# Kernel tuning notes

Hardware: AMD Instinct MI355X
Metric: run time of the kernel (lower is better)

## Reference

```python
import jax, jax.numpy as jnp
import numpy as np
from jax import lax

S = 8192      # total tokens
HID = 1280    # hidden_size
H = 16        # num_heads
D = HID // H  # head_dim = 80
NSEG = 8      # number of equal-length segments (images)


def rotate_half(x):
    half = x.shape[-1] // 2
    return jnp.concatenate([-x[..., half:], x[..., :half]], axis=-1)


def setup_inputs() -> dict:
    key = jax.random.key(0)
    k1, k2, k3, k4 = jax.random.split(key, 4)
    hidden_states = jax.random.normal(k1, (S, HID), dtype=jnp.float32)
    # rotary embeddings: angles repeated over both halves, as in standard vision RoPE
    theta = jax.random.uniform(k2, (S, D // 2), dtype=jnp.float32) * (2.0 * np.pi)
    freqs = jnp.concatenate([theta, theta], axis=-1)  # [S, D]
    cos = jnp.cos(freqs)
    sin = jnp.sin(freqs)
    qkv_kernel = jax.random.normal(k3, (HID, 3, H, D), dtype=jnp.float32) * 0.02
    qkv_bias = jnp.zeros((3, H, D), dtype=jnp.float32)
    proj_kernel = jax.random.normal(k4, (H * D, HID), dtype=jnp.float32) * 0.02
    proj_bias = jnp.zeros((HID,), dtype=jnp.float32)
    cu_seqlens = jnp.arange(NSEG + 1, dtype=jnp.int32) * (S // NSEG)
    return {
        "hidden_states": hidden_states, "cos": cos, "sin": sin,
        "qkv_kernel": qkv_kernel, "qkv_bias": qkv_bias,
        "proj_kernel": proj_kernel, "proj_bias": proj_bias,
        "cu_seqlens": cu_seqlens,
    }


def reference(hidden_states, cos, sin, qkv_kernel, qkv_bias, proj_kernel, proj_bias, cu_seqlens):
    P = lax.Precision.HIGHEST
    seq, dtype = hidden_states.shape[0], hidden_states.dtype
    # fused QKV projection: [S, 3, H, D]
    qkv = jnp.einsum('sd,dtnh->stnh', hidden_states, qkv_kernel, precision=P) + qkv_bias
    q, k, v = qkv[:, 0], qkv[:, 1], qkv[:, 2]
    # rotary position embedding in fp32 (as in original)
    cf = cos[:, None, :].astype(jnp.float32)
    sf = sin[:, None, :].astype(jnp.float32)
    qf = q.astype(jnp.float32)
    kf = k.astype(jnp.float32)
    q = (qf * cf + rotate_half(qf) * sf).astype(dtype)
    k = (kf * cf + rotate_half(kf) * sf).astype(dtype)
    # block-diagonal attention over equal-length segments from cu_seqlens
    n_seg = cu_seqlens.shape[0] - 1
    L = seq // n_seg  # segment length (uniform segments)
    head_dim = q.shape[-1]
    scale = head_dim ** (-0.5)
    qs = q.reshape(n_seg, L, H, head_dim)
    ks = k.reshape(n_seg, L, H, head_dim)
    vs = v.reshape(n_seg, L, H, head_dim)
    logits = jnp.einsum('bqhd,bkhd->bhqk', qs, ks, precision=P) * scale
    attn = jax.nn.softmax(logits.astype(jnp.float32), axis=-1).astype(dtype)
    out = jnp.einsum('bhqk,bkhd->bqhd', attn, vs, precision=P).reshape(seq, H * head_dim)
    return jnp.einsum('se,ed->sd', out, proj_kernel, precision=P) + proj_bias
```

## Files before the change

### kernel.cpp

```cpp
#include <hip/hip_runtime.h>

#define S_LEN 8192
#define HID   1280
#define NHEAD 16
#define HD    80
#define NQKV  3840
#define VTS   8256

#define GLOBAL_AS __attribute__((address_space(1)))
#define LDS_AS    __attribute__((address_space(3)))

typedef __attribute__((ext_vector_type(8))) short bf16x8;
typedef __attribute__((ext_vector_type(4))) float f32x4;
typedef __attribute__((ext_vector_type(4))) unsigned short u16x4;
typedef __attribute__((ext_vector_type(8))) unsigned short u16x8;
typedef __attribute__((ext_vector_type(2))) unsigned int u32x2;

__device__ __forceinline__ unsigned short f2bf(float f) {
    union { float f; unsigned int u; } v; v.f = f;
    unsigned int r = v.u + 0x7FFFu + ((v.u >> 16) & 1u);
    return (unsigned short)(r >> 16);
}
__device__ __forceinline__ float bf2f(unsigned short h) {
    union { unsigned int u; float f; } v; v.u = ((unsigned int)h) << 16;
    return v.f;
}
__device__ __forceinline__ unsigned int cvt_pk_bf16(float a, float b) {
    unsigned int r;
    asm("v_cvt_pk_bf16_f32 %0, %1, %2" : "=v"(r) : "v"(a), "v"(b));
    return r;
}

__global__ __launch_bounds__(256) void k_cvt(const float* __restrict__ src,
                                             unsigned short* __restrict__ dst, int n4)
{
    int i = blockIdx.x * 256 + threadIdx.x;
    if (i >= n4) return;
    f32x4 v = *(const f32x4*)&src[(size_t)i * 4];
    u16x4 o;
    o[0] = f2bf(v[0]); o[1] = f2bf(v[1]); o[2] = f2bf(v[2]); o[3] = f2bf(v[3]);
    *(u16x4*)&dst[(size_t)i * 4] = o;
}

__global__ __launch_bounds__(256) void k_wt(const float* __restrict__ W,
                                            unsigned short* __restrict__ Wt,
                                            int R, int C)
{
    __shared__ float T[32][33];
    int r0 = blockIdx.y * 32, c0 = blockIdx.x * 32;
    int tr = threadIdx.x >> 3, tc = (threadIdx.x & 7) * 4;
    f32x4 v = *(const f32x4*)&W[(size_t)(r0 + tr) * C + c0 + tc];
    T[tr][tc + 0] = v[0]; T[tr][tc + 1] = v[1];
    T[tr][tc + 2] = v[2]; T[tr][tc + 3] = v[3];
    __syncthreads();
    int c = threadIdx.x >> 3, r4 = (threadIdx.x & 7) * 4;
    u16x4 o;
    o[0] = f2bf(T[r4 + 0][c]); o[1] = f2bf(T[r4 + 1][c]);
    o[2] = f2bf(T[r4 + 2][c]); o[3] = f2bf(T[r4 + 3][c]);
    *(u16x4*)&Wt[(size_t)(c0 + c) * R + r0 + r4] = o;
}

__global__ __launch_bounds__(256) void k_vtr(const unsigned short* __restrict__ vb,
                                             unsigned short* __restrict__ vt)
{
    const int b = blockIdx.x;
    const int h = b >> 6, s0 = (b & 63) * 128;
    const int tid = threadIdx.x;
    if (tid >= 160) return;
    const int sblk = tid & 15, dch = tid >> 4;
    u16x8 a[8];
#pragma unroll
    for (int j = 0; j < 8; ++j)
        a[j] = *(const u16x8*)&vb[(size_t)(s0 + sblk * 8 + j) * HID + h * HD + dch * 8];
#pragma unroll
    for (int jj = 0; jj < 8; ++jj) {
        u16x8 o;
#pragma unroll
        for (int j = 0; j < 8; ++j) o[j] = a[j][jj];
        *(u16x8*)&vt[(size_t)(h * HD + dch * 8 + jj) * VTS + s0 + sblk * 8] = o;
    }
}

__global__ __launch_bounds__(512, 2) void k_qkv256(
    const unsigned short* __restrict__ A,
    const unsigned short* __restrict__ Bt,
    const float* __restrict__ bias,
    unsigned short* __restrict__ q0, unsigned short* __restrict__ k0p,
    unsigned short* __restrict__ v0)
{
    __shared__ __align__(16) unsigned short As[2][2][16][64][8];
    __shared__ __align__(16) unsigned short Bs[2][2][16][64][8];
    const int tid = threadIdx.x;
    const int w = tid >> 6, l = tid & 63;
    const int qg = l & 15, g = l >> 4;
    const int wm = w >> 2, wn = w & 3;
    const int wm8 = wm * 8, wn4 = wn * 4;

    const int bid = blockIdx.x;
    const int xcd = bid & 7, t = bid >> 3;
    const int bm0 = (xcd * 4 + (t & 3)) * 256;
    const int bn0 = (t >> 2) * 256;

    const unsigned short* ga = A + (size_t)(bm0 + w * 16 + qg) * HID + g * 8;
    const unsigned short* gb = Bt + (size_t)(bn0 + w * 16 + qg) * HID + g * 8;

#define SG_A(d, ks, kcol) do {                                                  \
    __builtin_amdgcn_global_load_lds((const GLOBAL_AS unsigned int*)(ga + (kcol)), \
        (LDS_AS unsigned int*)&As[d][ks][w][0][0], 16, 0, 0);                   \
    __builtin_amdgcn_global_load_lds((const GLOBAL_AS unsigned int*)(ga + (size_t)128 * HID + (kcol)), \
        (LDS_AS unsigned int*)&As[d][ks][8 + w][0][0], 16, 0, 0); } while (0)
#define SG_B(d, ks, kcol) do {                                                  \
    __builtin_amdgcn_global_load_lds((const GLOBAL_AS unsigned int*)(gb + (kcol)), \
        (LDS_AS unsigned int*)&Bs[d][ks][w][0][0], 16, 0, 0);                   \
    __builtin_amdgcn_global_load_lds((const GLOBAL_AS unsigned int*)(gb + (size_t)128 * HID + (kcol)), \
        (LDS_AS unsigned int*)&Bs[d][ks][8 + w][0][0], 16, 0, 0); } while (0)

#define RD_A4(d, ks, fb) do {                                                   \
    af[0] = *(const bf16x8*)&As[d][ks][wm8 + (fb) + 0][l][0];                   \
    af[1] = *(const bf16x8*)&As[d][ks][wm8 + (fb) + 1][l][0];                   \
    af[2] = *(const bf16x8*)&As[d][ks][wm8 + (fb) + 2][l][0];                   \
    af[3] = *(const bf16x8*)&As[d][ks][wm8 + (fb) + 3][l][0]; } while (0)
#define RD_B4(d, ks) do {                                                       \
    bf[0] = *(const bf16x8*)&Bs[d][ks][wn4 + 0][l][0];                          \
    bf[1] = *(const bf16x8*)&Bs[d][ks][wn4 + 1][l][0];                          \
    bf[2] = *(const bf16x8*)&Bs[d][ks][wn4 + 2][l][0];                          \
    bf[3] = *(const bf16x8*)&Bs[d][ks][wn4 + 3][l][0]; } while (0)

#define MFMAQ(base) do {                                                        \
    _Pragma("unroll")                                                           \
    for (int m = 0; m < 4; ++m)                                                 \
        _Pragma("unroll")                                                       \
        for (int n = 0; n < 4; ++n)                                             \
            acc[(base) + m][n] = __builtin_amdgcn_mfma_f32_16x16x32_bf16(       \
                af[m], bf[n], acc[(base) + m][n], 0, 0, 0); } while (0)

#define BARW() do { __builtin_amdgcn_s_barrier();                               \
    asm volatile("s_waitcnt lgkmcnt(0)" ::: "memory");                          \
    __builtin_amdgcn_sched_barrier(0);                                          \
    __builtin_amdgcn_s_setprio(1); } while (0)
#define BARC() do { __builtin_amdgcn_s_setprio(0);                              \
    __builtin_amdgcn_s_barrier();                                               \
    __builtin_amdgcn_sched_barrier(0); } while (0)
#define BARC_VM4() do { __builtin_amdgcn_s_setprio(0);                          \
    asm volatile("s_waitcnt vmcnt(4)" ::: "memory");                            \
    __builtin_amdgcn_s_barrier();                                               \
    __builtin_amdgcn_sched_barrier(0); } while (0)
#define BARC_VM0() do { __builtin_amdgcn_s_setprio(0);                          \
    asm volatile("s_waitcnt vmcnt(0)" ::: "memory");                            \
    __builtin_amdgcn_s_barrier();                                               \
    __builtin_amdgcn_sched_barrier(0); } while (0)

    f32x4 acc[8][4];
#pragma unroll
    for (int m = 0; m < 8; ++m)
#pragma unroll
        for (int n = 0; n < 4; ++n) acc[m][n] = (f32x4){0.f, 0.f, 0.f, 0.f};

    SG_A(0, 0, 0);  SG_B(0, 0, 0);
    SG_A(0, 1, 32); SG_B(0, 1, 32);
    SG_A(1, 0, 64); SG_B(1, 0, 64);
    asm volatile("s_waitcnt vmcnt(4)" ::: "memory");
    __builtin_amdgcn_s_barrier();
    __builtin_amdgcn_sched_barrier(0);

    const int NIT = HID / 128;
    for (int j = 0; j < NIT; ++j) {
        const bool st = (j + 1 < NIT);
        const int c1 = j * 128 + 96;
        const int c2 = j * 128 + 128;
        const int c2b = j * 128 + 160;
        const int c3 = j * 128 + 192;
        bf16x8 af[4], bf[4];

        RD_A4(0, 0, 0); RD_B4(0, 0);
        SG_A(1, 1, c1);
        BARW(); MFMAQ(0); BARC();
        RD_A4(0, 0, 4);
        SG_B(1, 1, c1);
        BARW(); MFMAQ(4); BARC();
        RD_A4(0, 1, 0); RD_B4(0, 1);
        if (st) SG_A(0, 0, c2);
        BARW(); MFMAQ(0); BARC();
        RD_A4(0, 1, 4);
        if (st) SG_B(0, 0, c2);
        BARW(); MFMAQ(4);
        if (st) BARC_VM4(); else BARC_VM0();
        RD_A4(1, 0, 0); RD_B4(1, 0);
        if (st) SG_A(0, 1, c2b);
        BARW(); MFMAQ(0); BARC();
        RD_A4(1, 0, 4);
        if (st) SG_B(0, 1, c2b);
        BARW(); MFMAQ(4); BARC();
        RD_A4(1, 1, 0); RD_B4(1, 1);
        if (st) SG_A(1, 0, c3);
        BARW(); MFMAQ(0); BARC();
        RD_A4(1, 1, 4);
        if (st) SG_B(1, 0, c3);
        BARW(); MFMAQ(4);
        if (st) BARC_VM4(); else BARC_VM0();
    }
#undef SG_A
#undef SG_B
#undef RD_A4
#undef RD_B4
#undef MFMAQ
#undef BARW
#undef BARC
#undef BARC_VM4
#undef BARC_VM0

    const int t3 = bn0 / HID;
    unsigned short* dst = (t3 == 0) ? q0 : ((t3 == 1) ? k0p : v0);
    const int colbase = bn0 - t3 * HID + wn * 64 + qg;
    float bv[4];
#pragma unroll
    for (int n = 0; n < 4; ++n) bv[n] = bias[bn0 + wn * 64 + n * 16 + qg];
#pragma unroll
    for (int m = 0; m < 8; ++m)
#pragma unroll
        for (int r = 0; r < 4; ++r) {
            const int row = bm0 + wm * 128 + m * 16 + g * 4 + r;
            unsigned short* drow = dst + (size_t)row * HID + colbase;
#pragma unroll
            for (int n = 0; n < 4; ++n)
                drow[n * 16] = f2bf(acc[m][n][r] + bv[n]);
        }
}

__global__ __launch_bounds__(256) void k_rope(
    unsigned short* __restrict__ qb, unsigned short* __restrict__ kb,
    const float* __restrict__ cosb, const float* __restrict__ sinb)
{
    const float SCQ = 0.11180339887498949f * 1.44269504088896340f;
    int idx = blockIdx.x * 256 + threadIdx.x;
    if (idx >= S_LEN * NHEAD * 10) return;
    int s = idx / 160;
    int rem = idx - s * 160;
    int nh = rem / 10, h4 = (rem - nh * 10) * 4;
    size_t base = (size_t)s * HID + nh * HD + h4;
    f32x4 c0 = *(const f32x4*)&cosb[s * HD + h4];
    f32x4 c1 = *(const f32x4*)&cosb[s * HD + h4 + 40];
    f32x4 s0 = *(const f32x4*)&sinb[s * HD + h4];
    f32x4 s1 = *(const f32x4*)&sinb[s * HD + h4 + 40];
    u16x4 qa = *(const u16x4*)&qb[base];
    u16x4 qb4 = *(const u16x4*)&qb[base + 40];
    u16x4 ka = *(const u16x4*)&kb[base];
    u16x4 kb4 = *(const u16x4*)&kb[base + 40];
    u16x4 o0, o1, p0, p1;
#pragma unroll
    for (int j = 0; j < 4; ++j) {
        float qaf = bf2f(qa[j]), qbf = bf2f(qb4[j]);
        o0[j] = f2bf((qaf * c0[j] - qbf * s0[j]) * SCQ);
        o1[j] = f2bf((qbf * c1[j] + qaf * s1[j]) * SCQ);
        float kaf = bf2f(ka[j]), kbf = bf2f(kb4[j]);
        p0[j] = f2bf(kaf * c0[j] - kbf * s0[j]);
        p1[j] = f2bf(kbf * c1[j] + kaf * s1[j]);
    }
    *(u16x4*)&qb[base] = o0;
    *(u16x4*)&qb[base + 40] = o1;
    *(u16x4*)&kb[base] = p0;
    *(u16x4*)&kb[base + 40] = p1;
}

__global__ __launch_bounds__(256) void k_attn(
    const unsigned short* __restrict__ qb, const unsigned short* __restrict__ kbuf,
    const unsigned short* __restrict__ vt, unsigned short* __restrict__ ao)
{
    __shared__ __align__(16) unsigned short Ks[2][64][104];
    __shared__ __align__(16) unsigned short Vs[2][80][64];
    __shared__ __align__(16) unsigned short Pls[4][2][16][68];

    const int tid = threadIdx.x;
    const int w = tid >> 6, l = tid & 63;
    const int qg = l & 15, g = l >> 4;
    const int wb = w << 6;
    const int vxor = (qg & 7) << 4;

    const int b = blockIdx.x;
    const int xcd = b & 7, j = b >> 3;
    const int p = xcd * 16 + (j >> 3);
    const int qt = j & 7;
    const int seg = p >> 4, head = p & 15;
    const int row0 = seg * 1024 + qt * 128 + w * 32;
    const size_t hoff = (size_t)head * HD;
    const int vhead = head * HD;
    const int kb0 = seg * 1024;

#define STAGE(bi, kr0_)                                                        \
    {                                                                          \
        const int kr0s = (kr0_);                                               \
        _Pragma("unroll")                                                      \
        for (int i = 0; i < 4; ++i) {                                          \
            const int u = i * 256 + tid;                                       \
            if (u < 832) {                                                     \
                const int r = u / 13, cu = (u - r * 13) * 8;                   \
                __builtin_amdgcn_global_load_lds(                              \
                    (const GLOBAL_AS unsigned int*)&kbuf[(size_t)(kr0s + r) * HID + hoff + cu], \
                    (LDS_AS unsigned int*)((LDS_AS unsigned short*)&Ks[bi][0][0] + (size_t)(i * 256 + wb) * 8), \
                    16, 0, 0);                                                 \
            }                                                                  \
        }                                                                      \
        _Pragma("unroll")                                                      \
        for (int i = 0; i < 3; ++i) {                                          \
            const int u = i * 256 + tid;                                       \
            if (u < 640) {                                                     \
                const int r = u >> 3;                                          \
                const int cs = ((u & 7) * 16) ^ ((r & 7) << 4);                \
                __builtin_amdgcn_global_load_lds(                              \
                    (const GLOBAL_AS unsigned int*)&vt[(size_t)(vhead + r) * VTS + kr0s + (cs >> 1)], \
                    (LDS_AS unsigned int*)((LDS_AS unsigned short*)&Vs[bi][0][0] + (size_t)(i * 256 + wb) * 8), \
                    16, 0, 0);                                                 \
            }                                                                  \
        }                                                                      \
    }

#define COMPUTE(bi)                                                            \
    {                                                                          \
        f32x4 st[2][4];                                                        \
        _Pragma("unroll")                                                      \
        for (int s = 0; s < 2; ++s)                                            \
            _Pragma("unroll")                                                  \
            for (int kn = 0; kn < 4; ++kn) st[s][kn] = (f32x4){0.f, 0.f, 0.f, 0.f}; \
        _Pragma("unroll")                                                      \
        for (int ks = 0; ks < 3; ++ks)                                         \
            _Pragma("unroll")                                                  \
            for (int kn = 0; kn < 4; ++kn) {                                   \
                bf16x8 kf = *(const bf16x8*)&Ks[bi][kn * 16 + qg][ks * 32 + g * 8]; \
                st[0][kn] = __builtin_amdgcn_mfma_f32_16x16x32_bf16(kf, qf[0][ks], st[0][kn], 0, 0, 0); \
                st[1][kn] = __builtin_amdgcn_mfma_f32_16x16x32_bf16(kf, qf[1][ks], st[1][kn], 0, 0, 0); \
            }                                                                  \
        _Pragma("unroll")                                                      \
        for (int s = 0; s < 2; ++s) {                                          \
            float psum = 0.f;                                                  \
            _Pragma("unroll")                                                  \
            for (int kn = 0; kn < 4; ++kn) {                                   \
                float p0 = exp2f(st[s][kn][0]);                                \
                float p1 = exp2f(st[s][kn][1]);                                \
                float p2 = exp2f(st[s][kn][2]);                                \
                float p3 = exp2f(st[s][kn][3]);                                \
                psum += (p0 + p1) + (p2 + p3);                                 \
                u32x2 pk;                                                      \
                pk[0] = cvt_pk_bf16(p0, p1);                                   \
                pk[1] = cvt_pk_bf16(p2, p3);                                   \
                *(u32x2*)&Pls[w][s][qg][kn * 16 + g * 4] = pk;                 \
            }                                                                  \
            psum += __shfl_xor(psum, 16, 64);                                  \
            psum += __shfl_xor(psum, 32, 64);                                  \
            lsum[s] += psum;                                                   \
        }                                                                      \
        _Pragma("unroll")                                                      \
        for (int ks = 0; ks < 2; ++ks) {                                       \
            bf16x8 pf0 = *(const bf16x8*)&Pls[w][0][qg][ks * 32 + g * 8];      \
            bf16x8 pf1 = *(const bf16x8*)&Pls[w][1][qg][ks * 32 + g * 8];      \
            _Pragma("unroll")                                                  \
            for (int d = 0; d < 5; ++d) {                                      \
                bf16x8 vf = *(const bf16x8*)((const unsigned short*)&Vs[bi][0][0] + \
                    (d * 16 + qg) * 64 + (((ks * 64 + g * 16) ^ vxor) >> 1));  \
                acc[0][d] = __builtin_amdgcn_mfma_f32_16x16x32_bf16(vf, pf0, acc[0][d], 0, 0, 0); \
                acc[1][d] = __builtin_amdgcn_mfma_f32_16x16x32_bf16(vf, pf1, acc[1][d], 0, 0, 0); \
            }                                                                  \
        }                                                                      \
    }

    bf16x8 qf[2][3];
#pragma unroll
    for (int s = 0; s < 2; ++s)
#pragma unroll
        for (int ks = 0; ks < 3; ++ks) {
            if (ks < 2 || g < 2)
                qf[s][ks] = *(const bf16x8*)&qb[(size_t)(row0 + s * 16 + qg) * HID + hoff + ks * 32 + g * 8];
            else
                qf[s][ks] = (bf16x8)(short)0;
        }

    float lsum[2] = {0.f, 0.f};
    f32x4 acc[2][5];
#pragma unroll
    for (int s = 0; s < 2; ++s)
#pragma unroll
        for (int d = 0; d < 5; ++d) acc[s][d] = (f32x4){0.f, 0.f, 0.f, 0.f};

    STAGE(0, kb0);
    __syncthreads();
    for (int ch = 0; ch < 16; ch += 2) {
        if (ch + 1 < 16) STAGE(1, kb0 + (ch + 1) * 64);
        COMPUTE(0);
        __syncthreads();
        if (ch + 2 < 16) STAGE(0, kb0 + (ch + 2) * 64);
        COMPUTE(1);
        __syncthreads();
    }

#pragma unroll
    for (int s = 0; s < 2; ++s) {
        const float inv = 1.0f / lsum[s];
        const int orow = row0 + s * 16 + qg;
#pragma unroll
        for (int d = 0; d < 5; ++d) {
            u16x4 o;
#pragma unroll
            for (int r = 0; r < 4; ++r) o[r] = f2bf(acc[s][d][r] * inv);
            *(u16x4*)&ao[(size_t)orow * HID + hoff + d * 16 + g * 4] = o;
        }
    }
#undef STAGE
#undef COMPUTE
}

__global__ __launch_bounds__(256) void k_proj(
    const unsigned short* __restrict__ A,
    const unsigned short* __restrict__ Bt,
    const float* __restrict__ bias, float* __restrict__ out)
{
    __shared__ __align__(16) unsigned short As[128][32];
    __shared__ __align__(16) unsigned short Bs[128][32];
    const int tid = threadIdx.x;
    const int w = tid >> 6, l = tid & 63;
    const int qg = l & 15, g = l >> 4;
    const int wr = w >> 1, wc = w & 1;
    const int bid = blockIdx.x;
    const int xcd = bid & 7, t = bid >> 3;
    const int bm0 = (xcd * 8 + (t & 7)) * 128;
    const int bn0 = (t >> 3) * 128;

    f32x4 acc[4][4];
#pragma unroll
    for (int m = 0; m < 4; ++m)
#pragma unroll
        for (int n = 0; n < 4; ++n) acc[m][n] = (f32x4){0.f, 0.f, 0.f, 0.f};

    const int lr = l >> 2, lc = (l & 3) * 8;
    const unsigned short* ga = A + (size_t)(bm0 + w * 16 + lr) * HID + lc;
    const unsigned short* gb = Bt + (size_t)(bn0 + w * 16 + lr) * HID + lc;
    LDS_AS unsigned int* la0 = (LDS_AS unsigned int*)&As[w * 16][0];
    LDS_AS unsigned int* la1 = (LDS_AS unsigned int*)&As[w * 16 + 64][0];
    LDS_AS unsigned int* lb0 = (LDS_AS unsigned int*)&Bs[w * 16][0];
    LDS_AS unsigned int* lb1 = (LDS_AS unsigned int*)&Bs[w * 16 + 64][0];

    for (int k0 = 0; k0 < HID; k0 += 32) {
        __syncthreads();
        __builtin_amdgcn_global_load_lds((const GLOBAL_AS unsigned int*)(ga + k0), la0, 16, 0, 0);
        __builtin_amdgcn_global_load_lds((const GLOBAL_AS unsigned int*)(ga + (size_t)64 * HID + k0), la1, 16, 0, 0);
        __builtin_amdgcn_global_load_lds((const GLOBAL_AS unsigned int*)(gb + k0), lb0, 16, 0, 0);
        __builtin_amdgcn_global_load_lds((const GLOBAL_AS unsigned int*)(gb + (size_t)64 * HID + k0), lb1, 16, 0, 0);
        __syncthreads();
        bf16x8 af[4], bff[4];
#pragma unroll
        for (int m = 0; m < 4; ++m) af[m] = *(const bf16x8*)&As[wr * 64 + m * 16 + qg][g * 8];
#pragma unroll
        for (int n = 0; n < 4; ++n) bff[n] = *(const bf16x8*)&Bs[wc * 64 + n * 16 + qg][g * 8];
#pragma unroll
        for (int m = 0; m < 4; ++m)
#pragma unroll
            for (int n = 0; n < 4; ++n)
                acc[m][n] = __builtin_amdgcn_mfma_f32_16x16x32_bf16(af[m], bff[n], acc[m][n], 0, 0, 0);
    }

#pragma unroll
    for (int n = 0; n < 4; ++n) {
        const int col = bn0 + wc * 64 + n * 16 + qg;
        const float bv = bias[col];
#pragma unroll
        for (int m = 0; m < 4; ++m)
#pragma unroll
            for (int r = 0; r < 4; ++r) {
                const int row = bm0 + wr * 64 + m * 16 + g * 4 + r;
                out[(size_t)row * HID + col] = acc[m][n][r] + bv;
            }
    }
}

extern "C" void kernel_launch(void* const* d_in, const int* in_sizes, int n_in,
                              void* d_out, int out_size, void* d_ws, size_t ws_size,
                              hipStream_t stream)
{
    (void)in_sizes; (void)n_in; (void)out_size; (void)ws_size;
    const float* hidden = (const float*)d_in[0];
    const float* cosb   = (const float*)d_in[1];
    const float* sinb   = (const float*)d_in[2];
    const float* qkv_w  = (const float*)d_in[3];
    const float* qkv_b  = (const float*)d_in[4];
    const float* proj_w = (const float*)d_in[5];
    const float* proj_b = (const float*)d_in[6];

    float* out = (float*)d_out;
    unsigned short* ws = (unsigned short*)d_ws;
    const size_t n = (size_t)S_LEN * HID;
    unsigned short* hb     = ws;
    unsigned short* wqkvt  = hb + n;
    unsigned short* wprojt = wqkvt + (size_t)NQKV * HID;
    unsigned short* qb     = wprojt + (size_t)HID * HID;
    unsigned short* kb     = qb + n;
    unsigned short* vb     = kb + n;
    unsigned short* vt     = vb + n;
    unsigned short* aob    = vt + (size_t)NHEAD * HD * VTS;

    k_cvt<<<(int)((n / 4 + 255) / 256), 256, 0, stream>>>(hidden, hb, (int)(n / 4));
    dim3 gw1(NQKV / 32, HID / 32);
    k_wt<<<gw1, 256, 0, stream>>>(qkv_w, wqkvt, HID, NQKV);
    dim3 gw2(HID / 32, HID / 32);
    k_wt<<<gw2, 256, 0, stream>>>(proj_w, wprojt, HID, HID);

    k_qkv256<<<480, 512, 0, stream>>>(hb, wqkvt, qkv_b, qb, kb, vb);

    k_rope<<<(S_LEN * NHEAD * 10 + 255) / 256, 256, 0, stream>>>(qb, kb, cosb, sinb);

    k_vtr<<<NHEAD * (S_LEN / 128), 256, 0, stream>>>(vb, vt);

    k_attn<<<1024, 256, 0, stream>>>(qb, kb, vt, aob);

    k_proj<<<640, 256, 0, stream>>>(aob, wprojt, proj_b, out);
}
```

Baseline: 257.2 us.

## Write V transposed from QKV GEMM epilogue and drop separate transpose kernel

The QKV GEMM epilogue now writes the V third of its output directly in transposed [head_dim][seq] layout into the vt buffer. This removes the k_vtr launch and its round trip of V through global memory. The attention kernel also gains s_setprio hints that raise wave priority around its MFMA blocks. k_cvt zeroes a small vb region, apparently to keep some padding initialized, and the transposed epilogue stores are column-strided and may coalesce less well.

```diff
diff --git a/kernel.cpp b/kernel.cpp
--- a/kernel.cpp
+++ b/kernel.cpp
@@ -32,9 +32,12 @@
 }
 
 __global__ __launch_bounds__(256) void k_cvt(const float* __restrict__ src,
-                                             unsigned short* __restrict__ dst, int n4)
+                                             unsigned short* __restrict__ dst,
+                                             unsigned short* __restrict__ vbz, int n4)
 {
     int i = blockIdx.x * 256 + threadIdx.x;
+    if (blockIdx.x == 0 && threadIdx.x < 4)
+        ((u16x8*)vbz)[threadIdx.x] = (u16x8)(unsigned short)0;
     if (i >= n4) return;
     f32x4 v = *(const f32x4*)&src[(size_t)i * 4];
     u16x4 o;
@@ -60,33 +63,12 @@
     *(u16x4*)&Wt[(size_t)(c0 + c) * R + r0 + r4] = o;
 }
 
-__global__ __launch_bounds__(256) void k_vtr(const unsigned short* __restrict__ vb,
-                                             unsigned short* __restrict__ vt)
-{
-    const int b = blockIdx.x;
-    const int h = b >> 6, s0 = (b & 63) * 128;
-    const int tid = threadIdx.x;
-    if (tid >= 160) return;
-    const int sblk = tid & 15, dch = tid >> 4;
-    u16x8 a[8];
-#pragma unroll
-    for (int j = 0; j < 8; ++j)
-        a[j] = *(const u16x8*)&vb[(size_t)(s0 + sblk * 8 + j) * HID + h * HD + dch * 8];
-#pragma unroll
-    for (int jj = 0; jj < 8; ++jj) {
-        u16x8 o;
-#pragma unroll
-        for (int j = 0; j < 8; ++j) o[j] = a[j][jj];
-        *(u16x8*)&vt[(size_t)(h * HD + dch * 8 + jj) * VTS + s0 + sblk * 8] = o;
-    }
-}
-
 __global__ __launch_bounds__(512, 2) void k_qkv256(
     const unsigned short* __restrict__ A,
     const unsigned short* __restrict__ Bt,
     const float* __restrict__ bias,
     unsigned short* __restrict__ q0, unsigned short* __restrict__ k0p,
-    unsigned short* __restrict__ v0)
+    unsigned short* __restrict__ vt)
 {
     __shared__ __align__(16) unsigned short As[2][2][16][64][8];
     __shared__ __align__(16) unsigned short Bs[2][2][16][64][8];
@@ -210,21 +192,38 @@
 #undef BARC_VM0
 
     const int t3 = bn0 / HID;
-    unsigned short* dst = (t3 == 0) ? q0 : ((t3 == 1) ? k0p : v0);
-    const int colbase = bn0 - t3 * HID + wn * 64 + qg;
-    float bv[4];
-#pragma unroll
-    for (int n = 0; n < 4; ++n) bv[n] = bias[bn0 + wn * 64 + n * 16 + qg];
-#pragma unroll
-    for (int m = 0; m < 8; ++m)
-#pragma unroll
-        for (int r = 0; r < 4; ++r) {
-            const int row = bm0 + wm * 128 + m * 16 + g * 4 + r;
-            unsigned short* drow = dst + (size_t)row * HID + colbase;
-#pragma unroll
-            for (int n = 0; n < 4; ++n)
-                drow[n * 16] = f2bf(acc[m][n][r] + bv[n]);
+    if (t3 < 2) {
+        unsigned short* dst = (t3 == 0) ? q0 : k0p;
+        const int colbase = bn0 - t3 * HID + wn * 64 + qg;
+        float bv[4];
+#pragma unroll
+        for (int n = 0; n < 4; ++n) bv[n] = bias[bn0 + wn * 64 + n * 16 + qg];
+#pragma unroll
+        for (int m = 0; m < 8; ++m)
+#pragma unroll
+            for (int r = 0; r < 4; ++r) {
+                const int row = bm0 + wm * 128 + m * 16 + g * 4 + r;
+                unsigned short* drow = dst + (size_t)row * HID + colbase;
+#pragma unroll
+                for (int n = 0; n < 4; ++n)
+                    drow[n * 16] = f2bf(acc[m][n][r] + bv[n]);
+            }
+    } else {
+        const int colbase = bn0 - 2 * HID + wn * 64;
+#pragma unroll
+        for (int n = 0; n < 4; ++n) {
+            const int vcol = colbase + n * 16 + qg;
+            const float bv = bias[bn0 + wn * 64 + n * 16 + qg];
+            unsigned short* dcol = vt + (size_t)vcol * VTS + bm0 + wm * 128 + g * 4;
+#pragma unroll
+            for (int m = 0; m < 8; ++m) {
+                u16x4 o;
+#pragma unroll
+                for (int r = 0; r < 4; ++r) o[r] = f2bf(acc[m][n][r] + bv);
+                *(u16x4*)&dcol[m * 16] = o;
+            }
         }
+    }
 }
 
 __global__ __launch_bounds__(256) void k_rope(
@@ -321,6 +320,7 @@
         for (int s = 0; s < 2; ++s)                                            \
             _Pragma("unroll")                                                  \
             for (int kn = 0; kn < 4; ++kn) st[s][kn] = (f32x4){0.f, 0.f, 0.f, 0.f}; \
+        __builtin_amdgcn_s_setprio(1);                                         \
         _Pragma("unroll")                                                      \
         for (int ks = 0; ks < 3; ++ks)                                         \
             _Pragma("unroll")                                                  \
@@ -329,6 +329,7 @@
                 st[0][kn] = __builtin_amdgcn_mfma_f32_16x16x32_bf16(kf, qf[0][ks], st[0][kn], 0, 0, 0); \
                 st[1][kn] = __builtin_amdgcn_mfma_f32_16x16x32_bf16(kf, qf[1][ks], st[1][kn], 0, 0, 0); \
             }                                                                  \
+        __builtin_amdgcn_s_setprio(0);                                         \
         _Pragma("unroll")                                                      \
         for (int s = 0; s < 2; ++s) {                                          \
             float psum = 0.f;                                                  \
@@ -348,6 +349,7 @@
             psum += __shfl_xor(psum, 32, 64);                                  \
             lsum[s] += psum;                                                   \
         }                                                                      \
+        __builtin_amdgcn_s_setprio(1);                                         \
         _Pragma("unroll")                                                      \
         for (int ks = 0; ks < 2; ++ks) {                                       \
             bf16x8 pf0 = *(const bf16x8*)&Pls[w][0][qg][ks * 32 + g * 8];      \
@@ -360,6 +362,7 @@
                 acc[1][d] = __builtin_amdgcn_mfma_f32_16x16x32_bf16(vf, pf1, acc[1][d], 0, 0, 0); \
             }                                                                  \
         }                                                                      \
+        __builtin_amdgcn_s_setprio(0);                                         \
     }
 
     bf16x8 qf[2][3];
@@ -495,18 +498,16 @@
     unsigned short* vt     = vb + n;
     unsigned short* aob    = vt + (size_t)NHEAD * HD * VTS;
 
-    k_cvt<<<(int)((n / 4 + 255) / 256), 256, 0, stream>>>(hidden, hb, (int)(n / 4));
+    k_cvt<<<(int)((n / 4 + 255) / 256), 256, 0, stream>>>(hidden, hb, vb, (int)(n / 4));
     dim3 gw1(NQKV / 32, HID / 32);
     k_wt<<<gw1, 256, 0, stream>>>(qkv_w, wqkvt, HID, NQKV);
     dim3 gw2(HID / 32, HID / 32);
     k_wt<<<gw2, 256, 0, stream>>>(proj_w, wprojt, HID, HID);
 
-    k_qkv256<<<480, 512, 0, stream>>>(hb, wqkvt, qkv_b, qb, kb, vb);
+    k_qkv256<<<480, 512, 0, stream>>>(hb, wqkvt, qkv_b, qb, kb, vt);
 
     k_rope<<<(S_LEN * NHEAD * 10 + 255) / 256, 256, 0, stream>>>(qb, kb, cosb, sinb);
 
-    k_vtr<<<NHEAD * (S_LEN / 128), 256, 0, stream>>>(vb, vt);
-
     k_attn<<<1024, 256, 0, stream>>>(qb, kb, vt, aob);
 
     k_proj<<<640, 256, 0, stream>>>(aob, wprojt, proj_b, out);
```

Result: no change. 255.3 us (-0.7%).
